# Kernel tuning notes

Hardware: AMD Instinct MI355X
Metric: run time of the kernel (lower is better)

The kernel has to match this reference:

```python
import jax, jax.numpy as jnp
import numpy as np

N = 4194304  # number of points (== number of edges)
M = 16384    # number of clusters


def setup_inputs() -> dict:
    key = jax.random.key(0)
    k1, k2, k3, k4, k5, k6 = jax.random.split(key, 6)
    x = jax.random.normal(k1, (N, 3), dtype=jnp.float32)
    pos = jax.random.normal(k2, (N, 3), dtype=jnp.float32)
    batch = jnp.zeros((N,), dtype=jnp.int64)
    cluster_weights = jax.random.uniform(k3, (M, 1), dtype=jnp.float32)
    R = jax.random.normal(k4, (M, 3, 3), dtype=jnp.float32)
    t = jax.random.normal(k5, (M, 3), dtype=jnp.float32)
    point_idx = jnp.arange(N, dtype=jnp.int64)
    cluster_idx = jax.random.randint(k6, (N,), 0, M, dtype=jnp.int64)
    edge_index = jnp.stack([point_idx, cluster_idx], axis=0)
    return {"x": x, "pos": pos, "batch": batch,
            "cluster_weights": cluster_weights, "R": R, "t": t,
            "edge_index": edge_index}


def reference(x, pos, batch, cluster_weights, R, t, edge_index):
    cluster_idx = edge_index[1]
    # gather per-edge rotation / translation / weight
    R_point = R[cluster_idx]            # [N, 3, 3]
    t_point = t[cluster_idx]            # [N, 3]
    # tiny batched 3x3 matmul + add
    x_pred = jnp.einsum('eij,ej->ei', R_point, pos) + t_point  # [N, 3]
    point_weights = cluster_weights[cluster_idx]               # [N, 1]
    x_out = x * point_weights + x_pred * (1.0 - point_weights)
    return (R_point, t_point, x_out)
```

## Files before the change

kernel.cpp:

```cpp
#include <hip/hip_runtime.h>


typedef float f4 __attribute__((ext_vector_type(4)));

__global__ void __launch_bounds__(256)
transf_prop_kernel(const float* __restrict__ x,
                   const float* __restrict__ pos,
                   const float* __restrict__ cw,
                   const float* __restrict__ Rm,
                   const float* __restrict__ tm,
                   const int*   __restrict__ cidx,
                   float* __restrict__ Rp,
                   float* __restrict__ tp,
                   float* __restrict__ xo,
                   int n)
{
    __shared__ __align__(16) float s_pos[768];
    __shared__ __align__(16) float s_x[768];
    __shared__ __align__(16) float s_R[2304];
    __shared__ __align__(16) float s_t[768];
    __shared__ __align__(16) float s_o[768];

    const int t    = threadIdx.x;
    const int base = blockIdx.x * 256;

    if (base + 256 <= n) {
        const int c = cidx[base + t];
        const float* Rc = Rm + (size_t)c * 9;
        float r[9];
        #pragma unroll
        for (int j = 0; j < 9; ++j) r[j] = Rc[j];
        const float* tc = tm + (size_t)c * 3;
        const float t0 = tc[0], t1 = tc[1], t2 = tc[2];
        const float w  = cw[c];

        const f4* pos4 = (const f4*)(pos + (size_t)base * 3);
        const f4* x4   = (const f4*)(x   + (size_t)base * 3);
        if (t < 192) {
            ((f4*)s_pos)[t] = pos4[t];
            ((f4*)s_x)[t]   = x4[t];
        }
        __syncthreads();

        const float p0 = s_pos[t * 3 + 0];
        const float p1 = s_pos[t * 3 + 1];
        const float p2 = s_pos[t * 3 + 2];
        const float x0 = s_x[t * 3 + 0];
        const float x1 = s_x[t * 3 + 1];
        const float x2 = s_x[t * 3 + 2];

        const float pr0 = fmaf(r[0], p0, fmaf(r[1], p1, fmaf(r[2], p2, t0)));
        const float pr1 = fmaf(r[3], p0, fmaf(r[4], p1, fmaf(r[5], p2, t1)));
        const float pr2 = fmaf(r[6], p0, fmaf(r[7], p1, fmaf(r[8], p2, t2)));
        const float omw = 1.0f - w;

        #pragma unroll
        for (int j = 0; j < 9; ++j) s_R[t * 9 + j] = r[j];
        s_t[t * 3 + 0] = t0;
        s_t[t * 3 + 1] = t1;
        s_t[t * 3 + 2] = t2;
        s_o[t * 3 + 0] = fmaf(x0, w, pr0 * omw);
        s_o[t * 3 + 1] = fmaf(x1, w, pr1 * omw);
        s_o[t * 3 + 2] = fmaf(x2, w, pr2 * omw);
        __syncthreads();

        f4* Rb4 = (f4*)(Rp + (size_t)base * 9);
        const f4* sR4 = (const f4*)s_R;
        __builtin_nontemporal_store(sR4[t],       &Rb4[t]);
        __builtin_nontemporal_store(sR4[t + 256], &Rb4[t + 256]);
        if (t < 64)
            __builtin_nontemporal_store(sR4[t + 512], &Rb4[t + 512]);

        f4* tb4 = (f4*)(tp + (size_t)base * 3);
        f4* ob4 = (f4*)(xo + (size_t)base * 3);
        if (t < 192) {
            __builtin_nontemporal_store(((const f4*)s_t)[t], &tb4[t]);
            __builtin_nontemporal_store(((const f4*)s_o)[t], &ob4[t]);
        }
    } else {
        const int m  = n - base;
        const int m3 = m * 3, m9 = m * 9;
        const float* posb = pos + (size_t)base * 3;
        const float* xb   = x   + (size_t)base * 3;
        for (int k = 0; k < 3; ++k) {
            int i = t + 256 * k;
            if (i < m3) { s_pos[i] = posb[i]; s_x[i] = xb[i]; }
        }
        __syncthreads();
        if (t < m) {
            const int c = cidx[base + t];
            const float* Rc = Rm + (size_t)c * 9;
            float r[9];
            for (int j = 0; j < 9; ++j) r[j] = Rc[j];
            const float* tc = tm + (size_t)c * 3;
            const float t0 = tc[0], t1 = tc[1], t2 = tc[2];
            const float w  = cw[c];
            const float p0 = s_pos[t*3], p1 = s_pos[t*3+1], p2 = s_pos[t*3+2];
            const float x0 = s_x[t*3],   x1 = s_x[t*3+1],   x2 = s_x[t*3+2];
            const float pr0 = fmaf(r[0], p0, fmaf(r[1], p1, fmaf(r[2], p2, t0)));
            const float pr1 = fmaf(r[3], p0, fmaf(r[4], p1, fmaf(r[5], p2, t1)));
            const float pr2 = fmaf(r[6], p0, fmaf(r[7], p1, fmaf(r[8], p2, t2)));
            const float omw = 1.0f - w;
            for (int j = 0; j < 9; ++j) s_R[t * 9 + j] = r[j];
            s_t[t*3] = t0; s_t[t*3+1] = t1; s_t[t*3+2] = t2;
            s_o[t*3]   = fmaf(x0, w, pr0 * omw);
            s_o[t*3+1] = fmaf(x1, w, pr1 * omw);
            s_o[t*3+2] = fmaf(x2, w, pr2 * omw);
        }
        __syncthreads();
        float* Rb = Rp + (size_t)base * 9;
        for (int k = 0; k < 9; ++k) {
            int i = t + 256 * k;
            if (i < m9) __builtin_nontemporal_store(s_R[i], &Rb[i]);
        }
        float* tb = tp + (size_t)base * 3;
        float* ob = xo + (size_t)base * 3;
        for (int k = 0; k < 3; ++k) {
            int i = t + 256 * k;
            if (i < m3) {
                __builtin_nontemporal_store(s_t[i], &tb[i]);
                __builtin_nontemporal_store(s_o[i], &ob[i]);
            }
        }
    }
}

extern "C" void kernel_launch(void* const* d_in, const int* in_sizes, int n_in,
                              void* d_out, int out_size, void* d_ws, size_t ws_size,
                              hipStream_t stream) {
    const float* x   = (const float*)d_in[0];
    const float* pos = (const float*)d_in[1];
    const float* cw  = (const float*)d_in[3];
    const float* Rm  = (const float*)d_in[4];
    const float* tm  = (const float*)d_in[5];
    const int*  edge = (const int*)d_in[6];

    const int n = in_sizes[0] / 3;
    const int* cidx = edge + n;

    float* out = (float*)d_out;
    float* Rp = out;
    float* tp = out + (size_t)n * 9;
    float* xo = out + (size_t)n * 12;

    const int block = 256;
    const int grid = (n + block - 1) / block;
    transf_prop_kernel<<<grid, block, 0, stream>>>(x, pos, cw, Rm, tm, cidx,
                                                   Rp, tp, xo, n);
}
```

Before: 77.21 us.

## Prepack per-cluster R, t, weight into aligned 64-byte rows for vector gathers

Adds a small prepass kernel that packs each cluster's 3x3 rotation, translation and weight into a 16-float row in workspace. The main kernel then gathers each cluster's parameters with four 16-byte vector loads from one aligned 64-byte row, replacing thirteen scalar loads spread over three arrays. This reduces the number of gather instructions and cache lines touched per point. The cost is an extra kernel launch and a small extra write and read of the packed table each call.

```diff
diff --git a/kernel.cpp b/kernel.cpp
--- a/kernel.cpp
+++ b/kernel.cpp
@@ -4,11 +4,26 @@
 typedef float f4 __attribute__((ext_vector_type(4)));
 
 __global__ void __launch_bounds__(256)
+prepack_kernel(const float* __restrict__ cw,
+               const float* __restrict__ Rm,
+               const float* __restrict__ tm,
+               float* __restrict__ packed,
+               int M)
+{
+    int i = blockIdx.x * 256 + threadIdx.x;
+    if (i >= M * 16) return;
+    int r = i >> 4, j = i & 15;
+    float v = 0.0f;
+    if (j < 9)       v = Rm[r * 9 + j];
+    else if (j < 12) v = tm[r * 3 + (j - 9)];
+    else if (j == 12) v = cw[r];
+    packed[i] = v;
+}
+
+__global__ void __launch_bounds__(256)
 transf_prop_kernel(const float* __restrict__ x,
                    const float* __restrict__ pos,
-                   const float* __restrict__ cw,
-                   const float* __restrict__ Rm,
-                   const float* __restrict__ tm,
+                   const float* __restrict__ packed,
                    const int*   __restrict__ cidx,
                    float* __restrict__ Rp,
                    float* __restrict__ tp,
@@ -26,13 +41,11 @@
 
     if (base + 256 <= n) {
         const int c = cidx[base + t];
-        const float* Rc = Rm + (size_t)c * 9;
-        float r[9];
-        #pragma unroll
-        for (int j = 0; j < 9; ++j) r[j] = Rc[j];
-        const float* tc = tm + (size_t)c * 3;
-        const float t0 = tc[0], t1 = tc[1], t2 = tc[2];
-        const float w  = cw[c];
+        const f4* row = (const f4*)(packed + (size_t)c * 16);
+        const f4 q0 = row[0];
+        const f4 q1 = row[1];
+        const f4 q2 = row[2];
+        const f4 q3 = row[3];
 
         const f4* pos4 = (const f4*)(pos + (size_t)base * 3);
         const f4* x4   = (const f4*)(x   + (size_t)base * 3);
@@ -49,16 +62,18 @@
         const float x1 = s_x[t * 3 + 1];
         const float x2 = s_x[t * 3 + 2];
 
-        const float pr0 = fmaf(r[0], p0, fmaf(r[1], p1, fmaf(r[2], p2, t0)));
-        const float pr1 = fmaf(r[3], p0, fmaf(r[4], p1, fmaf(r[5], p2, t1)));
-        const float pr2 = fmaf(r[6], p0, fmaf(r[7], p1, fmaf(r[8], p2, t2)));
+        const float pr0 = fmaf(q0.x, p0, fmaf(q0.y, p1, fmaf(q0.z, p2, q2.y)));
+        const float pr1 = fmaf(q0.w, p0, fmaf(q1.x, p1, fmaf(q1.y, p2, q2.z)));
+        const float pr2 = fmaf(q1.z, p0, fmaf(q1.w, p1, fmaf(q2.x, p2, q2.w)));
+        const float w   = q3.x;
         const float omw = 1.0f - w;
 
-        #pragma unroll
-        for (int j = 0; j < 9; ++j) s_R[t * 9 + j] = r[j];
-        s_t[t * 3 + 0] = t0;
-        s_t[t * 3 + 1] = t1;
-        s_t[t * 3 + 2] = t2;
+        s_R[t * 9 + 0] = q0.x; s_R[t * 9 + 1] = q0.y; s_R[t * 9 + 2] = q0.z;
+        s_R[t * 9 + 3] = q0.w; s_R[t * 9 + 4] = q1.x; s_R[t * 9 + 5] = q1.y;
+        s_R[t * 9 + 6] = q1.z; s_R[t * 9 + 7] = q1.w; s_R[t * 9 + 8] = q2.x;
+        s_t[t * 3 + 0] = q2.y;
+        s_t[t * 3 + 1] = q2.z;
+        s_t[t * 3 + 2] = q2.w;
         s_o[t * 3 + 0] = fmaf(x0, w, pr0 * omw);
         s_o[t * 3 + 1] = fmaf(x1, w, pr1 * omw);
         s_o[t * 3 + 2] = fmaf(x2, w, pr2 * omw);
@@ -89,12 +104,11 @@
         __syncthreads();
         if (t < m) {
             const int c = cidx[base + t];
-            const float* Rc = Rm + (size_t)c * 9;
+            const float* row = packed + (size_t)c * 16;
             float r[9];
-            for (int j = 0; j < 9; ++j) r[j] = Rc[j];
-            const float* tc = tm + (size_t)c * 3;
-            const float t0 = tc[0], t1 = tc[1], t2 = tc[2];
-            const float w  = cw[c];
+            for (int j = 0; j < 9; ++j) r[j] = row[j];
+            const float t0 = row[9], t1 = row[10], t2 = row[11];
+            const float w  = row[12];
             const float p0 = s_pos[t*3], p1 = s_pos[t*3+1], p2 = s_pos[t*3+2];
             const float x0 = s_x[t*3],   x1 = s_x[t*3+1],   x2 = s_x[t*3+2];
             const float pr0 = fmaf(r[0], p0, fmaf(r[1], p1, fmaf(r[2], p2, t0)));
@@ -136,6 +150,7 @@
     const int*  edge = (const int*)d_in[6];
 
     const int n = in_sizes[0] / 3;
+    const int M = in_sizes[3];
     const int* cidx = edge + n;
 
     float* out = (float*)d_out;
@@ -143,8 +158,13 @@
     float* tp = out + (size_t)n * 9;
     float* xo = out + (size_t)n * 12;
 
+    float* packed = (float*)d_ws;
+
     const int block = 256;
+    const int pgrid = (M * 16 + block - 1) / block;
+    prepack_kernel<<<pgrid, block, 0, stream>>>(cw, Rm, tm, packed, M);
+
     const int grid = (n + block - 1) / block;
-    transf_prop_kernel<<<grid, block, 0, stream>>>(x, pos, cw, Rm, tm, cidx,
+    transf_prop_kernel<<<grid, block, 0, stream>>>(x, pos, packed, cidx,
                                                    Rp, tp, xo, n);
 }
```

After: 63.25 us. 1.22x faster.
